# Performance work log

Hardware: AMD Instinct MI355X
Metric: run time of the kernel (lower is better)

## Reference

```python
import jax, jax.numpy as jnp
import numpy as np
from jax import lax

B, C, H, W = 4, 256, 64, 64
EPS = 1e-5  # BatchNorm eps (eval mode)


def _bn(x, g, b, m, v):
    # eval-mode BatchNorm2d over channel dim
    inv = lax.rsqrt(v + EPS)
    return (x - m[None, :, None, None]) * (g * inv)[None, :, None, None] + b[None, :, None, None]


def _conv1x1(x, w, b):
    # w: [O, I]
    return jnp.einsum('oc,bchw->bohw', w, x) + b[None, :, None, None]


def _conv3x3(x, w, b):
    # w: [O, I, 3, 3], padding 'same'
    y = lax.conv_general_dilated(x, w, (1, 1), 'SAME',
                                 dimension_numbers=('NCHW', 'OIHW', 'NCHW'))
    return y + b[None, :, None, None]


def setup_inputs():
    key = jax.random.key(0)
    ks = jax.random.split(key, 12)
    s = 0.05
    Ch = C // 2
    d = {
        'inputs_0': jax.random.normal(ks[0], (B, C, H, W), jnp.float32),
        'inputs_1': jax.random.normal(ks[1], (B, C, H, W), jnp.float32),
        # 1x1 projections (conv0/conv1/conv2): C -> C/2
        'w_q': jax.random.normal(ks[2], (Ch, C), jnp.float32) * s,
        'b_q': jnp.zeros((Ch,), jnp.float32),
        'w_k': jax.random.normal(ks[3], (Ch, C), jnp.float32) * s,
        'b_k': jnp.zeros((Ch,), jnp.float32),
        'w_v': jax.random.normal(ks[4], (Ch, C), jnp.float32) * s,
        'b_v': jnp.zeros((Ch,), jnp.float32),
        # conv3: C/2 -> C (1x1)
        'w_o': jax.random.normal(ks[5], (C, Ch), jnp.float32) * s,
        'b_o': jnp.zeros((C,), jnp.float32),
        # batch_conv0
        'bn0_g': jnp.ones((C,), jnp.float32), 'bn0_b': jnp.zeros((C,), jnp.float32),
        'bn0_m': jnp.zeros((C,), jnp.float32), 'bn0_v': jnp.ones((C,), jnp.float32),
        # conv_block(2C -> C): conv0 3x3
        'cb_w0': jax.random.normal(ks[6], (C, 2 * C, 3, 3), jnp.float32) * s,
        'cb_b0': jnp.zeros((C,), jnp.float32),
        'cb_bn0_g': jnp.ones((C,), jnp.float32), 'cb_bn0_b': jnp.zeros((C,), jnp.float32),
        'cb_bn0_m': jnp.zeros((C,), jnp.float32), 'cb_bn0_v': jnp.ones((C,), jnp.float32),
        # conv_block conv1 3x3: C -> C
        'cb_w1': jax.random.normal(ks[7], (C, C, 3, 3), jnp.float32) * s,
        'cb_b1': jnp.zeros((C,), jnp.float32),
        'cb_bn1_g': jnp.ones((C,), jnp.float32), 'cb_bn1_b': jnp.zeros((C,), jnp.float32),
        'cb_bn1_m': jnp.zeros((C,), jnp.float32), 'cb_bn1_v': jnp.ones((C,), jnp.float32),
    }
    return d


def reference(inputs_0, inputs_1, w_q, b_q, w_k, b_k, w_v, b_v, w_o, b_o,
              bn0_g, bn0_b, bn0_m, bn0_v,
              cb_w0, cb_b0, cb_bn0_g, cb_bn0_b, cb_bn0_m, cb_bn0_v,
              cb_w1, cb_b1, cb_bn1_g, cb_bn1_b, cb_bn1_m, cb_bn1_v):
    b, c, h, w = inputs_0.shape
    ch = c // 2
    n = h * w
    # 1x1 projections
    x1 = _conv1x1(inputs_0, w_q, b_q).reshape(b, ch, n)   # conv0(inputs_0)
    x2 = _conv1x1(inputs_0, w_k, b_k).reshape(b, ch, n)   # conv1(inputs_0)
    x3 = _conv1x1(inputs_1, w_v, b_v).reshape(b, ch, n)   # conv2(inputs_1)
    # spatial cross-attention: [b, n, n] affinity, contraction over channels
    aff = jnp.einsum('bij,bik->bjk', x2, x3)              # [b, n, n]
    aff = jax.nn.softmax(aff, axis=-2)                    # softmax over dim j (rows)
    x0 = jnp.einsum('bij,bjk->bik', x1, aff)              # [b, ch, n]
    x0 = x0.reshape(b, ch, h, w)
    # output projection + BN + GELU (exact erf gelu, matching torch default)
    x0 = jax.nn.gelu(_bn(_conv1x1(x0, w_o, b_o), bn0_g, bn0_b, bn0_m, bn0_v), approximate=False)
    # conv_block on concat
    y = jnp.concatenate([x0, inputs_0], axis=1)           # [b, 2c, h, w]
    y = jax.nn.gelu(_bn(_conv3x3(y, cb_w0, cb_b0), cb_bn0_g, cb_bn0_b, cb_bn0_m, cb_bn0_v), approximate=False)
    y = jax.nn.gelu(_bn(_conv3x3(y, cb_w1, cb_b1), cb_bn1_g, cb_bn1_b, cb_bn1_m, cb_bn1_v), approximate=False)
    # AdaptiveMaxPool2d((1,1)) == global spatial max, then squeeze -> [b, c]
    out = jnp.max(y + x0, axis=(2, 3))
    return out
```

## Files before the change

### kernel.cpp

```cpp
#include <hip/hip_runtime.h>
#include <math.h>

#define B_ 4
#define C_ 256
#define CH_ 128
#define NN 4096

typedef __bf16 bf16x8 __attribute__((ext_vector_type(8)));
typedef float f32x16 __attribute__((ext_vector_type(16)));
typedef unsigned int u32;

__device__ __forceinline__ float gelu_erf(float x) {
    return 0.5f * x * (1.0f + erff(x * 0.7071067811865476f));
}

__device__ __forceinline__ u32 pkbf(float a, float b) {
    union { __bf16 h[2]; u32 u; } x;
    x.h[0] = (__bf16)a; x.h[1] = (__bf16)b;
    return x.u;
}

__global__ __launch_bounds__(256) void nhwc_cast_kernel(
    const float* __restrict__ src, __bf16* __restrict__ dst,
    int colbase, int rowstride)
{
    __shared__ float Lt[64][65];
    const int t = threadIdx.x;
    const int p0 = blockIdx.x * 64;
    const int c0 = blockIdx.y * 64;
    const int b  = blockIdx.z;
#pragma unroll
    for (int i = 0; i < 16; ++i) {
        int idx = t + i * 256;
        int c = idx >> 6, p = idx & 63;
        Lt[c][p] = src[((size_t)(b * 256 + c0 + c)) * 4096 + p0 + p];
    }
    __syncthreads();
#pragma unroll
    for (int i = 0; i < 16; ++i) {
        int idx = t + i * 256;
        int p = idx >> 6, c = idx & 63;
        dst[((size_t)(b * 4096 + p0 + p)) * rowstride + colbase + c0 + c] = (__bf16)Lt[c][p];
    }
}

__global__ __launch_bounds__(256) void wtrans_kernel(
    const float* __restrict__ w0, const float* __restrict__ w1,
    const float* __restrict__ wq, const float* __restrict__ wk,
    const float* __restrict__ wv, const float* __restrict__ wo,
    __bf16* __restrict__ Wt0, __bf16* __restrict__ Wt1,
    __bf16* __restrict__ wqb, __bf16* __restrict__ wkb,
    __bf16* __restrict__ wvb, __bf16* __restrict__ wob)
{
    int id = blockIdx.x * 256 + threadIdx.x;
    if (id < 131072) {
        int o = id >> 9, ci = id & 511;
        const float* s = w0 + (size_t)id * 9;
        const int chunk = ci >> 4, f = o >> 5;
        const int lane = (o & 31) + 32 * ((ci >> 3) & 1);
        const int j = ci & 7;
#pragma unroll
        for (int k = 0; k < 9; ++k)
            Wt0[((size_t)(chunk * 9 + k) * 8 + f) * 512 + lane * 8 + j] = (__bf16)s[k];
    } else if (id < 196608) {
        int id2 = id - 131072;
        int o = id2 >> 8, ci = id2 & 255;
        const float* s = w1 + (size_t)id2 * 9;
        const int chunk = ci >> 4, f = o >> 5;
        const int lane = (o & 31) + 32 * ((ci >> 3) & 1);
        const int j = ci & 7;
#pragma unroll
        for (int k = 0; k < 9; ++k)
            Wt1[((size_t)(chunk * 9 + k) * 8 + f) * 512 + lane * 8 + j] = (__bf16)s[k];
    } else {
        int id3 = id - 196608;
        int sel = id3 >> 15;
        int k = id3 & 32767;
        const float* s = sel == 0 ? wq : sel == 1 ? wk : sel == 2 ? wv : wo;
        __bf16* d = sel == 0 ? wqb : sel == 1 ? wkb : sel == 2 ? wvb : wob;
        d[k] = (__bf16)s[k];
    }
}

__global__ __launch_bounds__(256) void proj_mfma_kernel(
    const __bf16* __restrict__ Xt0,
    const __bf16* __restrict__ Xin1,
    const __bf16* __restrict__ wqb, const __bf16* __restrict__ wkb,
    const __bf16* __restrict__ wvb,
    const float* __restrict__ bq, const float* __restrict__ bk,
    const float* __restrict__ bv,
    __bf16* __restrict__ Vswz, __bf16* __restrict__ Kswz, __bf16* __restrict__ Qswz)
{
    __shared__ __align__(16) __bf16 Vt[4][64][80];
    __shared__ float biasl[128];

    const int t = threadIdx.x;
    const int which = blockIdx.z % 3;
    const int b = blockIdx.z / 3;
    const int p0 = blockIdx.x * 128;

    const __bf16* W = which == 0 ? wqb : which == 1 ? wkb : wvb;
    const float* bias = which == 0 ? bq : which == 1 ? bk : bv;
    const __bf16* src; int stride, colb;
    if (which == 2) { src = Xin1 + (size_t)b * NN * 256; stride = 256; colb = 0; }
    else            { src = Xt0  + (size_t)b * NN * 512; stride = 512; colb = 256; }

    if (t < 128) biasl[t] = bias[t];
    __syncthreads();

    const int lane = t & 63, w = t >> 6;
    const int l31 = lane & 31, hi = lane >> 5;
    const int wo2 = w >> 1, wp2 = w & 1;
    const int ob = wo2 * 64;
    const int pb = p0 + wp2 * 64;

    f32x16 acc[2][2];
#pragma unroll
    for (int i = 0; i < 2; ++i)
#pragma unroll
        for (int j = 0; j < 2; ++j)
#pragma unroll
            for (int e = 0; e < 16; ++e) acc[i][j][e] = 0.f;

#pragma unroll
    for (int kc = 0; kc < 16; ++kc) {
        bf16x8 a0 = *(const bf16x8*)&W[(size_t)(ob + l31) * 256 + hi * 8 + kc * 16];
        bf16x8 a1 = *(const bf16x8*)&W[(size_t)(ob + 32 + l31) * 256 + hi * 8 + kc * 16];
        bf16x8 b0 = *(const bf16x8*)&src[(size_t)(pb + l31) * stride + colb + hi * 8 + kc * 16];
        bf16x8 b1 = *(const bf16x8*)&src[(size_t)(pb + 32 + l31) * stride + colb + hi * 8 + kc * 16];
        acc[0][0] = __builtin_amdgcn_mfma_f32_32x32x16_bf16(a0, b0, acc[0][0], 0, 0, 0);
        acc[0][1] = __builtin_amdgcn_mfma_f32_32x32x16_bf16(a0, b1, acc[0][1], 0, 0, 0);
        acc[1][0] = __builtin_amdgcn_mfma_f32_32x32x16_bf16(a1, b0, acc[1][0], 0, 0, 0);
        acc[1][1] = __builtin_amdgcn_mfma_f32_32x32x16_bf16(a1, b1, acc[1][1], 0, 0, 0);
    }

    if (which) {
        __bf16* dst = (which == 1 ? Kswz : Qswz) + (size_t)b * NN * CH_;
#pragma unroll
        for (int mi = 0; mi < 2; ++mi)
#pragma unroll
            for (int nx = 0; nx < 2; ++nx) {
                const int tile = (pb >> 5) + nx;
#pragma unroll
                for (int q4 = 0; q4 < 4; ++q4) {
                    const int ic = (ob >> 4) + mi * 2 + (q4 >> 1);
                    const int og = ob + mi * 32 + q4 * 8 + hi * 4;
                    __bf16 pk[4];
#pragma unroll
                    for (int j = 0; j < 4; ++j)
                        pk[j] = (__bf16)(acc[mi][nx][q4 * 4 + j] + biasl[og + j]);
                    const size_t el = ((size_t)(tile * 8 + ic) * 64
                                       + l31 + 32 * (q4 & 1)) * 8 + hi * 4;
                    *(uint2*)&dst[el] = *(const uint2*)pk;
                }
            }
    } else {
#pragma unroll
        for (int mi = 0; mi < 2; ++mi)
#pragma unroll
            for (int nx = 0; nx < 2; ++nx) {
                const int ploc = nx * 32 + l31;
#pragma unroll
                for (int q4 = 0; q4 < 4; ++q4) {
                    const int oloc = mi * 32 + q4 * 8 + hi * 4;
#pragma unroll
                    for (int j = 0; j < 4; ++j)
                        Vt[w][oloc + j][ploc] =
                            (__bf16)(acc[mi][nx][q4 * 4 + j] + biasl[ob + oloc + j]);
                }
            }
        __syncthreads();
        __bf16* dst = Vswz + (size_t)b * NN * CH_;
#pragma unroll
        for (int s = 0; s < 8; ++s) {
            const int tl = s >> 2, jc = (s >> 1) & 1, il = s & 1;
            const int tile_g = (pb >> 5) + tl;
            const int icf_g = (ob >> 5) + il;
            const int i_loc = il * 32 + l31;
            const int kk = tl * 32 + jc * 16 + hi * 8;
            uint4 v = *(const uint4*)&Vt[w][i_loc][kk];
            const size_t el = ((size_t)((tile_g * 2 + jc) * 4 + icf_g) * 64 + lane) * 8;
            *(uint4*)&dst[el] = v;
        }
    }
}

__global__ __launch_bounds__(256, 4) void attn_mfma_kernel(
    const __bf16* __restrict__ Qswz, const __bf16* __restrict__ Kswz,
    const __bf16* __restrict__ Vswz,
    __bf16* __restrict__ Opart, float* __restrict__ Mpart, float* __restrict__ Lpart)
{
    __shared__ __bf16 Op[4][128][34];
    __shared__ float Ml[4][32], Ll[4][32];

    const int t = threadIdx.x;
    const int lane = t & 63;
    const int w = t >> 6;
    const int l31 = lane & 31;
    const int hi = lane >> 5;

    const int bid = blockIdx.x;
    const int xcd = bid & 7;
    const int b = xcd >> 1;
    const int local = bid >> 3;
    const int qt = (xcd & 1) * 64 + (local & 63);
    const int half = local >> 6;
    const int q0 = qt * 32;

    const __bf16* Qs = Qswz + (size_t)b * NN * CH_ + (size_t)qt * 4096 + lane * 8;
    bf16x8 qf[8];
#pragma unroll
    for (int ic = 0; ic < 8; ++ic) qf[ic] = *(const bf16x8*)(Qs + ic * 512);

    const __bf16* Ks = Kswz + (size_t)b * NN * CH_ + lane * 8;
    const __bf16* Vs = Vswz + (size_t)b * NN * CH_ + lane * 8;

    f32x16 oacc[4];
#pragma unroll
    for (int i = 0; i < 4; ++i)
#pragma unroll
        for (int e = 0; e < 16; ++e) oacc[i][e] = 0.f;

    float m = -3e38f, lsum = 0.f;
    const int tbase = half * 64 + w * 16;

    for (int jt = 0; jt < 16; ++jt) {
        const int tile = tbase + jt;
        f32x16 s;
#pragma unroll
        for (int e = 0; e < 16; ++e) s[e] = 0.f;
        const __bf16* Kt = Ks + (size_t)tile * 4096;
#pragma unroll
        for (int ic = 0; ic < 8; ++ic) {
            bf16x8 kf = *(const bf16x8*)(Kt + ic * 512);
            s = __builtin_amdgcn_mfma_f32_32x32x16_bf16(kf, qf[ic], s, 0, 0, 0);
        }
        float t8[8];
#pragma unroll
        for (int e = 0; e < 8; ++e) t8[e] = fmaxf(s[e], s[e + 8]);
#pragma unroll
        for (int e = 0; e < 4; ++e) t8[e] = fmaxf(t8[e], t8[e + 4]);
        t8[0] = fmaxf(t8[0], t8[2]); t8[1] = fmaxf(t8[1], t8[3]);
        float mu = fmaxf(t8[0], t8[1]);
        const float pm = fmaxf(mu, __shfl_xor(mu, 32));
        if (!__all(pm <= m + 8.f)) {
            const float mn = fmaxf(m, pm);
            const float al = __expf(m - mn);
            m = mn;
            lsum *= al;
#pragma unroll
            for (int i = 0; i < 4; ++i)
#pragma unroll
                for (int e = 0; e < 16; ++e) oacc[i][e] *= al;
        }
#pragma unroll
        for (int e = 0; e < 16; ++e) s[e] = __expf(s[e] - m);
        float s8[8];
#pragma unroll
        for (int e = 0; e < 8; ++e) s8[e] = s[e] + s[e + 8];
#pragma unroll
        for (int e = 0; e < 4; ++e) s8[e] += s8[e + 4];
        s8[0] += s8[2]; s8[1] += s8[3];
        float su = s8[0] + s8[1];
        lsum += su + __shfl_xor(su, 32);

        const __bf16* Vt = Vs + (size_t)tile * 4096;
        {
            u32 w0 = pkbf(s[0], s[1]), w1 = pkbf(s[2], s[3]);
            u32 w2 = pkbf(s[4], s[5]), w3 = pkbf(s[6], s[7]);
            asm("v_permlane32_swap_b32 %0, %1" : "+v"(w0), "+v"(w2));
            asm("v_permlane32_swap_b32 %0, %1" : "+v"(w1), "+v"(w3));
            union { u32 u4[4]; bf16x8 v; } pB;
            pB.u4[0] = w0; pB.u4[1] = w1; pB.u4[2] = w2; pB.u4[3] = w3;
#pragma unroll
            for (int icf = 0; icf < 4; ++icf) {
                bf16x8 vf = *(const bf16x8*)(Vt + icf * 512);
                oacc[icf] = __builtin_amdgcn_mfma_f32_32x32x16_bf16(vf, pB.v, oacc[icf], 0, 0, 0);
            }
        }
        {
            u32 w0 = pkbf(s[8], s[9]), w1 = pkbf(s[10], s[11]);
            u32 w2 = pkbf(s[12], s[13]), w3 = pkbf(s[14], s[15]);
            asm("v_permlane32_swap_b32 %0, %1" : "+v"(w0), "+v"(w2));
            asm("v_permlane32_swap_b32 %0, %1" : "+v"(w1), "+v"(w3));
            union { u32 u4[4]; bf16x8 v; } pB;
            pB.u4[0] = w0; pB.u4[1] = w1; pB.u4[2] = w2; pB.u4[3] = w3;
#pragma unroll
            for (int icf = 0; icf < 4; ++icf) {
                bf16x8 vf = *(const bf16x8*)(Vt + 2048 + icf * 512);
                oacc[icf] = __builtin_amdgcn_mfma_f32_32x32x16_bf16(vf, pB.v, oacc[icf], 0, 0, 0);
            }
        }
    }

#pragma unroll
    for (int icf = 0; icf < 4; ++icf)
#pragma unroll
        for (int q = 0; q < 16; ++q) {
            const int row = icf * 32 + (q & 3) + 8 * (q >> 2) + 4 * hi;
            Op[w][row][l31] = (__bf16)oacc[icf][q];
        }
    if (hi == 0) { Ml[w][l31] = m; Ll[w][l31] = lsum; }
    __syncthreads();
    {
        const int q = t & 31;
        const int i0g = (t >> 5) * 16;
        const float m0 = Ml[0][q], m1 = Ml[1][q], m2 = Ml[2][q], m3 = Ml[3][q];
        const float ms = fmaxf(fmaxf(m0, m1), fmaxf(m2, m3));
        const float a0 = __expf(m0 - ms), a1 = __expf(m1 - ms);
        const float a2 = __expf(m2 - ms), a3 = __expf(m3 - ms);
        const float den = a0 * Ll[0][q] + a1 * Ll[1][q] + a2 * Ll[2][q] + a3 * Ll[3][q];
        union { __bf16 h[16]; uint4 u4[2]; } pk;
#pragma unroll
        for (int ii = 0; ii < 16; ++ii) {
            const int i = i0g + ii;
            pk.h[ii] = (__bf16)(a0 * (float)Op[0][i][q] + a1 * (float)Op[1][i][q]
                              + a2 * (float)Op[2][i][q] + a3 * (float)Op[3][i][q]);
        }
        const size_t base = ((size_t)((half * 4 + b) * NN) + q0 + q) * CH_ + i0g;
        *(uint4*)&Opart[base] = pk.u4[0];
        *(uint4*)&Opart[base + 8] = pk.u4[1];
        if (t < 32) {
            Mpart[(size_t)(half * 4 + b) * NN + q0 + q] = ms;
            Lpart[(size_t)(half * 4 + b) * NN + q0 + q] = den;
        }
    }
}

__global__ __launch_bounds__(256) void attn_merge_kernel(
    const __bf16* __restrict__ Opart, const float* __restrict__ Mpart,
    const float* __restrict__ Lpart, __bf16* __restrict__ x0)
{
    const int id = blockIdx.x * 256 + threadIdx.x;
    const int qg = id >> 2;
    const int i0 = (id & 3) * 32;
    const int b = qg >> 12, q = qg & 4095;
    const size_t idx0 = (size_t)b * NN + q;
    const size_t idx1 = (size_t)(4 + b) * NN + q;
    const float m0 = Mpart[idx0], m1 = Mpart[idx1];
    const float ms = fmaxf(m0, m1);
    const float a0 = __expf(m0 - ms), a1 = __expf(m1 - ms);
    const float inv = 1.f / (a0 * Lpart[idx0] + a1 * Lpart[idx1]);
    const __bf16* O0 = &Opart[idx0 * CH_ + i0];
    const __bf16* O1 = &Opart[idx1 * CH_ + i0];
    union { __bf16 h[32]; uint4 u4[4]; } ov;
#pragma unroll
    for (int ii = 0; ii < 32; ++ii)
        ov.h[ii] = (__bf16)((a0 * (float)O0[ii] + a1 * (float)O1[ii]) * inv);
    uint4* dst = (uint4*)&x0[((size_t)b * NN + q) * CH_ + i0];
#pragma unroll
    for (int s = 0; s < 4; ++s) dst[s] = ov.u4[s];
}

__global__ __launch_bounds__(256) void convo_mfma_kernel(
    const __bf16* __restrict__ x0, const __bf16* __restrict__ wob,
    const float* __restrict__ bo,
    const float* __restrict__ g, const float* __restrict__ bb,
    const float* __restrict__ mm, const float* __restrict__ vv,
    __bf16* __restrict__ Xt0)
{
    __shared__ float scb[128], shb[128], bsb[128];
    const int t = threadIdx.x;
    const int p0 = blockIdx.x * 128;
    const int o0 = blockIdx.y * 128;
    const int b = blockIdx.z;
    if (t < 128) {
        const int o = o0 + t;
        const float sc = g[o] * rsqrtf(vv[o] + 1e-5f);
        scb[t] = sc; shb[t] = bb[o] - mm[o] * sc; bsb[t] = bo[o];
    }
    __syncthreads();

    const int lane = t & 63, w = t >> 6;
    const int l31 = lane & 31, hi = lane >> 5;
    const int wo2 = w >> 1, wp2 = w & 1;
    const int ob = o0 + wo2 * 64;
    const int pb = p0 + wp2 * 64;

    f32x16 acc[2][2];
#pragma unroll
    for (int i = 0; i < 2; ++i)
#pragma unroll
        for (int j = 0; j < 2; ++j)
#pragma unroll
            for (int e = 0; e < 16; ++e) acc[i][j][e] = 0.f;

#pragma unroll
    for (int kc = 0; kc < 8; ++kc) {
        bf16x8 a0 = *(const bf16x8*)&wob[(size_t)(ob + l31) * 128 + hi * 8 + kc * 16];
        bf16x8 a1 = *(const bf16x8*)&wob[(size_t)(ob + 32 + l31) * 128 + hi * 8 + kc * 16];
        bf16x8 b0 = *(const bf16x8*)&x0[((size_t)(b * NN) + pb + l31) * 128 + hi * 8 + kc * 16];
        bf16x8 b1 = *(const bf16x8*)&x0[((size_t)(b * NN) + pb + 32 + l31) * 128 + hi * 8 + kc * 16];
        acc[0][0] = __builtin_amdgcn_mfma_f32_32x32x16_bf16(a0, b0, acc[0][0], 0, 0, 0);
        acc[0][1] = __builtin_amdgcn_mfma_f32_32x32x16_bf16(a0, b1, acc[0][1], 0, 0, 0);
        acc[1][0] = __builtin_amdgcn_mfma_f32_32x32x16_bf16(a1, b0, acc[1][0], 0, 0, 0);
        acc[1][1] = __builtin_amdgcn_mfma_f32_32x32x16_bf16(a1, b1, acc[1][1], 0, 0, 0);
    }

#pragma unroll
    for (int mi = 0; mi < 2; ++mi)
#pragma unroll
        for (int nx = 0; nx < 2; ++nx) {
            const int p = pb + nx * 32 + l31;
            const size_t rowbase = ((size_t)(b * NN) + p) * 512 + o0;
#pragma unroll
            for (int q4 = 0; q4 < 4; ++q4) {
                const int ol = wo2 * 64 + mi * 32 + q4 * 8 + hi * 4;
                __bf16 pk[4];
#pragma unroll
                for (int j = 0; j < 4; ++j) {
                    float v = acc[mi][nx][q4 * 4 + j] + bsb[ol + j];
                    v = v * scb[ol + j] + shb[ol + j];
                    pk[j] = (__bf16)gelu_erf(v);
                }
                *(uint2*)&Xt0[rowbase + ol] = *(const uint2*)pk;
            }
        }
}

template<int IC>
__global__ __launch_bounds__(128) void conv3x3_mfma_kernel(
    const __bf16* __restrict__ Xsrc,
    const __bf16* __restrict__ Wf,
    const float* __restrict__ bias, const float* __restrict__ bng,
    const float* __restrict__ bnb, const float* __restrict__ bnm,
    const float* __restrict__ bnv,
    __bf16* __restrict__ out)
{
    constexpr int NC2 = IC / 32;
    __shared__ __align__(16) char Tl[2][12672];
    __shared__ float scb[64], shb[64], bsb[64];

    const int t = threadIdx.x;
    const int bid = blockIdx.x;
    const int xcd = bid & 7, local = bid >> 3;
    const int combo = xcd * 2 + (local >> 6);
    const int y0 = local & 63;
    const int m = combo & 3, b = combo >> 2;
    const int o0 = m * 64;

    if (t < 64) {
        const int o = o0 + t;
        const float sc = bng[o] * rsqrtf(bnv[o] + 1e-5f);
        scb[t] = sc; shb[t] = bnb[o] - bnm[o] * sc; bsb[t] = bias[o];
    }

    const int lane = t & 63, w = t >> 6;
    const int l31 = lane & 31, hi = lane >> 5;

    uint4 ireg[6];

    auto loadI = [&](int c0) {
#pragma unroll
        for (int s = 0; s < 6; ++s) {
            int u = t + s * 128;
            int sl = u & 3, x = (u >> 2) & 63, r = u >> 8;
            int yy = y0 - 1 + r;
            if (yy >= 0 && yy < 64)
                ireg[s] = *(const uint4*)&Xsrc[((size_t)(b * 4096 + yy * 64 + x)) * IC + c0 + sl * 8];
            else
                ireg[s] = make_uint4(0u, 0u, 0u, 0u);
        }
    };
    auto writeI = [&](char* dst) {
#pragma unroll
        for (int s = 0; s < 6; ++s) {
            int u = t + s * 128;
            int sl = u & 3, x = (u >> 2) & 63, r = u >> 8;
            int xh = x + 1;
            int slot = (xh * 4 + sl) ^ (xh & 7);
            *(uint4*)(dst + r * 4224 + slot * 16) = ireg[s];
        }
        if (t < 24) {
            int sl = t & 3, side = (t >> 2) & 1, r = t >> 3;
            int xh = side ? 65 : 0;
            int slot = (xh * 4 + sl) ^ (xh & 7);
            *(uint4*)(dst + r * 4224 + slot * 16) = make_uint4(0u, 0u, 0u, 0u);
        }
    };

    const __bf16* Wb = Wf + ((size_t)(m * 2) * 64 + lane) * 8;
    bf16x8 wA[9][2][2];
    auto loadAk = [&](int cc, int k9) {
        const __bf16* wp0 = Wb + (size_t)((2 * cc) * 9 + k9) * 4096;
        const __bf16* wp1 = Wb + (size_t)((2 * cc + 1) * 9 + k9) * 4096;
        wA[k9][0][0] = *(const bf16x8*)(wp0);
        wA[k9][0][1] = *(const bf16x8*)(wp0 + 512);
        wA[k9][1][0] = *(const bf16x8*)(wp1);
        wA[k9][1][1] = *(const bf16x8*)(wp1 + 512);
    };

    f32x16 acc[2];
#pragma unroll
    for (int i = 0; i < 2; ++i)
#pragma unroll
        for (int e = 0; e < 16; ++e) acc[i][e] = 0.f;

    int Boff[3][2];
#pragma unroll
    for (int dx = 0; dx < 3; ++dx) {
        int xh = w * 32 + l31 + dx;
#pragma unroll
        for (int g = 0; g < 2; ++g)
            Boff[dx][g] = ((xh * 4 + g * 2 + hi) ^ (xh & 7)) * 16;
    }

    auto computePF = [&](const char* Tb, int ccNext) {
#pragma unroll
        for (int k9 = 0; k9 < 9; ++k9) {
            const int dy = k9 / 3, dx = k9 % 3;
            const char* Trow = Tb + dy * 4224;
            bf16x8 bv0 = *(const bf16x8*)(Trow + Boff[dx][0]);
            bf16x8 bv1 = *(const bf16x8*)(Trow + Boff[dx][1]);
            acc[0] = __builtin_amdgcn_mfma_f32_32x32x16_bf16(wA[k9][0][0], bv0, acc[0], 0, 0, 0);
            acc[1] = __builtin_amdgcn_mfma_f32_32x32x16_bf16(wA[k9][0][1], bv0, acc[1], 0, 0, 0);
            acc[0] = __builtin_amdgcn_mfma_f32_32x32x16_bf16(wA[k9][1][0], bv1, acc[0], 0, 0, 0);
            acc[1] = __builtin_amdgcn_mfma_f32_32x32x16_bf16(wA[k9][1][1], bv1, acc[1], 0, 0, 0);
            loadAk(ccNext, k9);
        }
    };

    loadI(0);
#pragma unroll
    for (int k9 = 0; k9 < 9; ++k9) loadAk(0, k9);
    writeI(Tl[0]);
    __syncthreads();
    for (int c = 0; c < NC2; ++c) {
        const int cur = c & 1;
        const int cn = (c + 1 < NC2) ? c + 1 : c;
        loadI(cn * 32);
        computePF(Tl[cur], cn);
        writeI(Tl[cur ^ 1]);
        __syncthreads();
    }

    {
        const int p = y0 * 64 + w * 32 + l31;
        const size_t rowbase = ((size_t)(b * 4096 + p)) * 256 + o0;
#pragma unroll
        for (int mi = 0; mi < 2; ++mi)
#pragma unroll
            for (int q = 0; q < 4; ++q) {
                const int obase = mi * 32 + q * 8 + hi * 4;
                __bf16 pk[4];
#pragma unroll
                for (int j = 0; j < 4; ++j) {
                    float v = acc[mi][q * 4 + j] + bsb[obase + j];
                    v = v * scb[obase + j] + shb[obase + j];
                    pk[j] = (__bf16)gelu_erf(v);
                }
                *(uint2*)&out[rowbase + obase] = *(const uint2*)pk;
            }
    }
}

__global__ __launch_bounds__(256) void maxpart_kernel(
    const __bf16* __restrict__ y1, const __bf16* __restrict__ xt0,
    float* __restrict__ part)
{
    const int o = threadIdx.x;
    const int chunk = blockIdx.x & 63;
    const int b = blockIdx.x >> 6;
    float mx = -1e30f;
    for (int pp = 0; pp < 64; ++pp) {
        int p = chunk * 64 + pp;
        float a = (float)y1[((size_t)(b * 4096 + p)) * 256 + o];
        float c = (float)xt0[((size_t)(b * 4096 + p)) * 512 + o];
        mx = fmaxf(mx, a + c);
    }
    part[((size_t)(b * 64 + chunk)) * 256 + o] = mx;
}

__global__ __launch_bounds__(256) void maxfin_kernel(
    const float* __restrict__ part, float* __restrict__ out)
{
    const int o = threadIdx.x;
    const int b = blockIdx.x;
    float mx = -1e30f;
    for (int c = 0; c < 64; ++c)
        mx = fmaxf(mx, part[((size_t)(b * 64 + c)) * 256 + o]);
    out[b * 256 + o] = mx;
}

extern "C" void kernel_launch(void* const* d_in, const int* in_sizes, int n_in,
                              void* d_out, int out_size, void* d_ws, size_t ws_size,
                              hipStream_t stream)
{
    const float* in0  = (const float*)d_in[0];
    const float* in1  = (const float*)d_in[1];
    const float* w_q  = (const float*)d_in[2];
    const float* b_q  = (const float*)d_in[3];
    const float* w_k  = (const float*)d_in[4];
    const float* b_k  = (const float*)d_in[5];
    const float* w_v  = (const float*)d_in[6];
    const float* b_v  = (const float*)d_in[7];
    const float* w_o  = (const float*)d_in[8];
    const float* b_o  = (const float*)d_in[9];
    const float* bn0g = (const float*)d_in[10];
    const float* bn0b = (const float*)d_in[11];
    const float* bn0m = (const float*)d_in[12];
    const float* bn0v = (const float*)d_in[13];
    const float* cbw0 = (const float*)d_in[14];
    const float* cbb0 = (const float*)d_in[15];
    const float* cb0g = (const float*)d_in[16];
    const float* cb0b = (const float*)d_in[17];
    const float* cb0m = (const float*)d_in[18];
    const float* cb0v = (const float*)d_in[19];
    const float* cbw1 = (const float*)d_in[20];
    const float* cbb1 = (const float*)d_in[21];
    const float* cb1g = (const float*)d_in[22];
    const float* cb1b = (const float*)d_in[23];
    const float* cb1m = (const float*)d_in[24];
    const float* cb1v = (const float*)d_in[25];

    char* wsb = (char*)d_ws;
    const size_t MB = 1u << 20;
    __bf16* Xt0  = (__bf16*)(wsb);
    __bf16* Xin1 = (__bf16*)(wsb + 16 * MB);
    __bf16* Opart= (__bf16*)(wsb + 16 * MB);
    __bf16* Qswz = (__bf16*)(wsb + 24 * MB);
    __bf16* x0   = (__bf16*)(wsb + 24 * MB);
    __bf16* Kswz = (__bf16*)(wsb + 28 * MB);
    __bf16* y0   = (__bf16*)(wsb + 24 * MB);
    __bf16* Vswz = (__bf16*)(wsb + 32 * MB);
    __bf16* y1   = (__bf16*)(wsb + 32 * MB);
    __bf16* wqb  = (__bf16*)(wsb + 40 * MB);
    __bf16* wkb  = (__bf16*)(wsb + 40 * MB + 65536);
    __bf16* wvb  = (__bf16*)(wsb + 40 * MB + 2 * 65536);
    __bf16* wob  = (__bf16*)(wsb + 40 * MB + 3 * 65536);
    __bf16* Wt0  = (__bf16*)(wsb + 40 * MB + 4 * 65536);
    __bf16* Wt1  = (__bf16*)(wsb + 40 * MB + 4 * 65536 + 2359296);
    float*  Mpart= (float*)(wsb + 44 * MB);
    float*  Lpart= (float*)(wsb + 44 * MB + 131072);
    float*  part = (float*)(wsb + 44 * MB + 2 * 131072);
    float* outp = (float*)d_out;

    nhwc_cast_kernel<<<dim3(64, 4, 4), 256, 0, stream>>>(in0, Xt0, 256, 512);
    nhwc_cast_kernel<<<dim3(64, 4, 4), 256, 0, stream>>>(in1, Xin1, 0, 256);
    wtrans_kernel<<<1280, 256, 0, stream>>>(cbw0, cbw1, w_q, w_k, w_v, w_o,
                                            Wt0, Wt1, wqb, wkb, wvb, wob);
    proj_mfma_kernel<<<dim3(32, 1, 12), 256, 0, stream>>>(
        Xt0, Xin1, wqb, wkb, wvb, b_q, b_k, b_v, Vswz, Kswz, Qswz);
    attn_mfma_kernel<<<1024, 256, 0, stream>>>(Qswz, Kswz, Vswz, Opart, Mpart, Lpart);
    attn_merge_kernel<<<256, 256, 0, stream>>>(Opart, Mpart, Lpart, x0);
    convo_mfma_kernel<<<dim3(32, 2, 4), 256, 0, stream>>>(
        x0, wob, b_o, bn0g, bn0b, bn0m, bn0v, Xt0);
    conv3x3_mfma_kernel<512><<<1024, 128, 0, stream>>>(Xt0, Wt0, cbb0, cb0g, cb0b, cb0m, cb0v, y0);
    conv3x3_mfma_kernel<256><<<1024, 128, 0, stream>>>(y0, Wt1, cbb1, cb1g, cb1b, cb1m, cb1v, y1);
    maxpart_kernel<<<256, 256, 0, stream>>>(y1, Xt0, part);
    maxfin_kernel<<<4, 256, 0, stream>>>(part, outp);
}
```

Before: 253.8 us.

## Split conv3x3 K-reduction across two wave groups with LDS merge

```diff
diff --git a/kernel.cpp b/kernel.cpp
--- a/kernel.cpp
+++ b/kernel.cpp
@@ -419,7 +419,7 @@
 }
 
 template<int IC>
-__global__ __launch_bounds__(128) void conv3x3_mfma_kernel(
+__global__ __launch_bounds__(256, 4) void conv3x3_mfma_kernel(
     const __bf16* __restrict__ Xsrc,
     const __bf16* __restrict__ Wf,
     const float* __restrict__ bias, const float* __restrict__ bng,
@@ -434,9 +434,9 @@
     const int t = threadIdx.x;
     const int bid = blockIdx.x;
     const int xcd = bid & 7, local = bid >> 3;
-    const int combo = xcd * 2 + (local >> 6);
-    const int y0 = local & 63;
-    const int m = combo & 3, b = combo >> 2;
+    const int b = xcd >> 1, yhi = xcd & 1;
+    const int y0 = yhi * 32 + (local & 31);
+    const int m = local >> 5;
     const int o0 = m * 64;
 
     if (t < 64) {
@@ -446,14 +446,17 @@
     }
 
     const int lane = t & 63, w = t >> 6;
+    const int g = w >> 1;
+    const int xh2 = w & 1;
     const int l31 = lane & 31, hi = lane >> 5;
 
-    uint4 ireg[6];
-
-    auto loadI = [&](int c0) {
-#pragma unroll
-        for (int s = 0; s < 6; ++s) {
-            int u = t + s * 128;
+    uint4 ireg[3];
+
+    auto loadI = [&](int cc) {
+        const int c0 = cc * 32;
+#pragma unroll
+        for (int s = 0; s < 3; ++s) {
+            int u = t + s * 256;
             int sl = u & 3, x = (u >> 2) & 63, r = u >> 8;
             int yy = y0 - 1 + r;
             if (yy >= 0 && yy < 64)
@@ -464,8 +467,8 @@
     };
     auto writeI = [&](char* dst) {
 #pragma unroll
-        for (int s = 0; s < 6; ++s) {
-            int u = t + s * 128;
+        for (int s = 0; s < 3; ++s) {
+            int u = t + s * 256;
             int sl = u & 3, x = (u >> 2) & 63, r = u >> 8;
             int xh = x + 1;
             int slot = (xh * 4 + sl) ^ (xh & 7);
@@ -480,14 +483,11 @@
     };
 
     const __bf16* Wb = Wf + ((size_t)(m * 2) * 64 + lane) * 8;
-    bf16x8 wA[9][2][2];
+    bf16x8 wA[9][2];
     auto loadAk = [&](int cc, int k9) {
-        const __bf16* wp0 = Wb + (size_t)((2 * cc) * 9 + k9) * 4096;
-        const __bf16* wp1 = Wb + (size_t)((2 * cc + 1) * 9 + k9) * 4096;
-        wA[k9][0][0] = *(const bf16x8*)(wp0);
-        wA[k9][0][1] = *(const bf16x8*)(wp0 + 512);
-        wA[k9][1][0] = *(const bf16x8*)(wp1);
-        wA[k9][1][1] = *(const bf16x8*)(wp1 + 512);
+        const __bf16* wp = Wb + (size_t)((2 * cc + g) * 9 + k9) * 4096;
+        wA[k9][0] = *(const bf16x8*)(wp);
+        wA[k9][1] = *(const bf16x8*)(wp + 512);
     };
 
     f32x16 acc[2];
@@ -496,26 +496,20 @@
 #pragma unroll
         for (int e = 0; e < 16; ++e) acc[i][e] = 0.f;
 
-    int Boff[3][2];
+    int Boff[3];
 #pragma unroll
     for (int dx = 0; dx < 3; ++dx) {
-        int xh = w * 32 + l31 + dx;
-#pragma unroll
-        for (int g = 0; g < 2; ++g)
-            Boff[dx][g] = ((xh * 4 + g * 2 + hi) ^ (xh & 7)) * 16;
+        int xh = xh2 * 32 + l31 + dx;
+        Boff[dx] = ((xh * 4 + g * 2 + hi) ^ (xh & 7)) * 16;
     }
 
     auto computePF = [&](const char* Tb, int ccNext) {
 #pragma unroll
         for (int k9 = 0; k9 < 9; ++k9) {
             const int dy = k9 / 3, dx = k9 % 3;
-            const char* Trow = Tb + dy * 4224;
-            bf16x8 bv0 = *(const bf16x8*)(Trow + Boff[dx][0]);
-            bf16x8 bv1 = *(const bf16x8*)(Trow + Boff[dx][1]);
-            acc[0] = __builtin_amdgcn_mfma_f32_32x32x16_bf16(wA[k9][0][0], bv0, acc[0], 0, 0, 0);
-            acc[1] = __builtin_amdgcn_mfma_f32_32x32x16_bf16(wA[k9][0][1], bv0, acc[1], 0, 0, 0);
-            acc[0] = __builtin_amdgcn_mfma_f32_32x32x16_bf16(wA[k9][1][0], bv1, acc[0], 0, 0, 0);
-            acc[1] = __builtin_amdgcn_mfma_f32_32x32x16_bf16(wA[k9][1][1], bv1, acc[1], 0, 0, 0);
+            bf16x8 bv = *(const bf16x8*)(Tb + dy * 4224 + Boff[dx]);
+            acc[0] = __builtin_amdgcn_mfma_f32_32x32x16_bf16(wA[k9][0], bv, acc[0], 0, 0, 0);
+            acc[1] = __builtin_amdgcn_mfma_f32_32x32x16_bf16(wA[k9][1], bv, acc[1], 0, 0, 0);
             loadAk(ccNext, k9);
         }
     };
@@ -528,14 +522,32 @@
     for (int c = 0; c < NC2; ++c) {
         const int cur = c & 1;
         const int cn = (c + 1 < NC2) ? c + 1 : c;
-        loadI(cn * 32);
+        if (c + 1 < NC2) loadI(c + 1);
         computePF(Tl[cur], cn);
-        writeI(Tl[cur ^ 1]);
         __syncthreads();
-    }
-
-    {
-        const int p = y0 * 64 + w * 32 + l31;
+        if (c + 1 < NC2) writeI(Tl[cur ^ 1]);
+        __syncthreads();
+    }
+
+    float* mrg = (float*)&Tl[0][0];
+    __syncthreads();
+    if (g == 1) {
+        const int idx = t - 128;
+#pragma unroll
+        for (int i = 0; i < 2; ++i)
+#pragma unroll
+            for (int e = 0; e < 16; ++e)
+                mrg[idx * 33 + i * 16 + e] = acc[i][e];
+    }
+    __syncthreads();
+    if (g == 0) {
+        const int idx = t;
+#pragma unroll
+        for (int i = 0; i < 2; ++i)
+#pragma unroll
+            for (int e = 0; e < 16; ++e)
+                acc[i][e] += mrg[idx * 33 + i * 16 + e];
+        const int p = y0 * 64 + xh2 * 32 + l31;
         const size_t rowbase = ((size_t)(b * 4096 + p)) * 256 + o0;
 #pragma unroll
         for (int mi = 0; mi < 2; ++mi)
@@ -645,8 +657,8 @@
     attn_merge_kernel<<<256, 256, 0, stream>>>(Opart, Mpart, Lpart, x0);
     convo_mfma_kernel<<<dim3(32, 2, 4), 256, 0, stream>>>(
         x0, wob, b_o, bn0g, bn0b, bn0m, bn0v, Xt0);
-    conv3x3_mfma_kernel<512><<<1024, 128, 0, stream>>>(Xt0, Wt0, cbb0, cb0g, cb0b, cb0m, cb0v, y0);
-    conv3x3_mfma_kernel<256><<<1024, 128, 0, stream>>>(y0, Wt1, cbb1, cb1g, cb1b, cb1m, cb1v, y1);
+    conv3x3_mfma_kernel<512><<<1024, 256, 0, stream>>>(Xt0, Wt0, cbb0, cb0g, cb0b, cb0m, cb0v, y0);
+    conv3x3_mfma_kernel<256><<<1024, 256, 0, stream>>>(y0, Wt1, cbb1, cb1g, cb1b, cb1m, cb1v, y1);
     maxpart_kernel<<<256, 256, 0, stream>>>(y1, Xt0, part);
     maxfin_kernel<<<4, 256, 0, stream>>>(part, outp);
 }
```

New measurement: 280.5 us. 1.1x slower.
